# Kernel tuning notes

Hardware: AMD Instinct MI355X
Metric: run time of the kernel (lower is better)

Reference implementation:

```python
import jax, jax.numpy as jnp
import numpy as np

P = 2        # patch_size
HEADS = 1


def _conv(x, w, b, groups=1):
    # NCHW conv, kernel 3x3, SAME padding (stride 1)
    y = jax.lax.conv_general_dilated(
        x, w, window_strides=(1, 1), padding='SAME',
        dimension_numbers=('NCHW', 'OIHW', 'NCHW'),
        feature_group_count=groups)
    return y + b[None, :, None, None]


def _unfold(x, p):
    # torch.nn.Unfold(kernel=p, stride=p): [B,C,h,w] -> [B, C*p*p, n]
    B, C, h, w = x.shape
    x = x.reshape(B, C, h // p, p, w // p, p)
    x = x.transpose(0, 1, 3, 5, 2, 4)  # (B, C, ph, pw, h/p, w/p)
    return x.reshape(B, C * p * p, (h // p) * (w // p))


def _fold(x, p, h, w):
    # inverse of _unfold (non-overlapping patches)
    B = x.shape[0]
    C = x.shape[1] // (p * p)
    x = x.reshape(B, C, p, p, h // p, w // p)
    x = x.transpose(0, 1, 4, 2, 5, 3)  # (B, C, h/p, ph, w/p, pw)
    return x.reshape(B, C, h, w)


def setup_inputs() -> dict:
    key = jax.random.key(0)
    ks = jax.random.split(key, 9)
    c = 64
    x = jax.random.normal(ks[0], (2, 5, c, 64, 64), jnp.float32)
    wq = jax.random.normal(ks[1], (c, 1, 3, 3), jnp.float32) * 0.1
    bq = jax.random.normal(ks[2], (c,), jnp.float32) * 0.1
    wk = jax.random.normal(ks[3], (c, 1, 3, 3), jnp.float32) * 0.1
    bk = jax.random.normal(ks[4], (c,), jnp.float32) * 0.1
    wv = jax.random.normal(ks[5], (c, c, 3, 3), jnp.float32) * 0.05
    bv = jax.random.normal(ks[6], (c,), jnp.float32) * 0.1
    wc = jax.random.normal(ks[7], (c, c, 3, 3), jnp.float32) * 0.05
    bc = jax.random.normal(ks[8], (c,), jnp.float32) * 0.1
    return {"x": x, "wq": wq, "bq": bq, "wk": wk, "bk": bk,
            "wv": wv, "bv": bv, "wc": wc, "bc": bc}


def reference(x, wq, bq, wk, bk, wv, bv, wc, bc):
    b, t, c, h, w = x.shape
    p, H = P, HEADS
    D = p * p * c           # 256
    d = D // H              # per-head dim
    n = (h // p) * (w // p)  # tokens per frame

    xf = x.reshape(b * t, c, h, w)
    q = _conv(xf, wq, bq, groups=c)   # depthwise
    k = _conv(xf, wk, bk, groups=c)   # depthwise
    v = _conv(xf, wv, bv)             # dense conv

    def to_tokens(y):
        # [bt, D, n] -> [b, H, d, t*n]
        u = _unfold(y, p).reshape(b, t, H, d, n)
        return u.transpose(0, 2, 3, 1, 4).reshape(b, H, d, t * n)

    uq, uk, uv = to_tokens(q), to_tokens(k), to_tokens(v)

    attn = jnp.einsum('bhdi,bhdj->bhij', uq, uk) * (d ** -0.5)
    attn = jax.nn.softmax(attn, axis=-1)           # [b,H,tn,tn]
    ax = jnp.einsum('bhij,bhdj->bhid', attn, uv)   # [b,H,tn,d]

    ax = ax.reshape(b, H, t, n, d).transpose(0, 2, 1, 4, 3).reshape(b * t, D, n)
    feat = _fold(ax, p, h, w)                      # [bt, c, h, w]
    out = _conv(feat, wc, bc).reshape(x.shape) + x
    return out
```

## Files before the change

kernel.cpp:

```cpp
#include <hip/hip_runtime.h>
#include <hip/hip_bf16.h>

typedef __attribute__((ext_vector_type(8))) short short8;
typedef __attribute__((ext_vector_type(8))) unsigned short ushort8;
typedef __attribute__((ext_vector_type(4))) unsigned short ushort4v;
typedef __attribute__((ext_vector_type(4))) float f32x4;

#define NTOK 5120
#define DDIM 256
#define NJC 8

__device__ __forceinline__ unsigned short f2bf(float f) {
  union { float f; unsigned int u; } x; x.f = f;
  unsigned int r = x.u + 0x7FFFu + ((x.u >> 16) & 1u);
  return (unsigned short)(r >> 16);
}
__device__ __forceinline__ float bf2f(unsigned short u) {
  union { unsigned int i; float f; } x; x.i = ((unsigned int)u) << 16; return x.f;
}

__global__ __launch_bounds__(256) void qk_gen(
    const float* __restrict__ xin, const float* __restrict__ wq,
    const float* __restrict__ bq, const float* __restrict__ wk,
    const float* __restrict__ bk, unsigned short* __restrict__ qt,
    unsigned short* __restrict__ kt)
{
  const int ch = blockIdx.x;
  const int bt = blockIdx.y;
  const int b = bt / 5, tf = bt % 5;
  const int tid = threadIdx.x;
  const float* xp = xin + ((size_t)bt * 64 + ch) * 4096;
  float wqv[9], wkv[9];
  #pragma unroll
  for (int i = 0; i < 9; i++) { wqv[i] = wq[ch * 9 + i]; wkv[i] = wk[ch * 9 + i]; }
  const float bqv = bq[ch], bkv = bk[ch];

  #pragma unroll
  for (int p = 0; p < 4; p++) {
    int pid = tid + p * 256;
    int gy = pid >> 5, gx = pid & 31;
    float v[4][4];
    #pragma unroll
    for (int r = 0; r < 4; r++) {
      int yy = 2 * gy - 1 + r;
      #pragma unroll
      for (int cc = 0; cc < 4; cc++) {
        int xx = 2 * gx - 1 + cc;
        bool ok = (yy >= 0) && (yy < 64) && (xx >= 0) && (xx < 64);
        v[r][cc] = ok ? xp[yy * 64 + xx] : 0.f;
      }
    }
    unsigned short qo[4], ko[4];
    #pragma unroll
    for (int py = 0; py < 2; py++)
      #pragma unroll
      for (int px = 0; px < 2; px++) {
        float aq = bqv, ak = bkv;
        #pragma unroll
        for (int dy = 0; dy < 3; dy++)
          #pragma unroll
          for (int dx = 0; dx < 3; dx++) {
            float xv = v[py + dy][px + dx];
            aq += wqv[dy * 3 + dx] * xv;
            ak += wkv[dy * 3 + dx] * xv;
          }
        qo[py * 2 + px] = f2bf(aq);
        ko[py * 2 + px] = f2bf(ak);
      }
    size_t base = ((size_t)(b * NTOK + tf * 1024 + pid)) * DDIM + ch * 4;
    ushort4v qv = { qo[0], qo[1], qo[2], qo[3] };
    ushort4v kv = { ko[0], ko[1], ko[2], ko[3] };
    *(ushort4v*)(qt + base) = qv;
    *(ushort4v*)(kt + base) = kv;
  }
}

__global__ __launch_bounds__(256) void wt_gen(
    const float* __restrict__ w0, const float* __restrict__ w1,
    unsigned short* __restrict__ o0, unsigned short* __restrict__ o1)
{
  const int tap = blockIdx.x;
  const float* src = blockIdx.y ? w1 : w0;
  unsigned short* dst = blockIdx.y ? o1 : o0;
  const int t = threadIdx.x;
  #pragma unroll
  for (int i = 0; i < 16; i++) {
    int oi = t + i * 256;
    dst[tap * 4096 + oi] = f2bf(src[(size_t)oi * 9 + tap]);
  }
}

template<int MODE>
__global__ __launch_bounds__(256) void conv_mfma(
    const float* __restrict__ src, const unsigned short* __restrict__ wt,
    const float* __restrict__ bias, const float* __restrict__ resid,
    float* __restrict__ dstf, unsigned short* __restrict__ vt)
{
  const int strip = blockIdx.x;
  const int bt = blockIdx.y;
  const int y0 = strip * 2;
  const int tid = threadIdx.x;
  const int sw = tid >> 6, lane = tid & 63;
  const int ry = sw >> 1, ch = sw & 1;
  const int g = lane >> 4, c = lane & 15;

  __shared__ __align__(16) unsigned short lds_in[4 * 66 * 64];
  __shared__ __align__(16) unsigned short lds_w[64 * 64];

  {
    const int rr = lane >> 4;
    const int cb = lane & 15;
    const int row = y0 - 1 + rr;
    const bool rok = (row >= 0) && (row < 64);
    #pragma unroll
    for (int pp = 0; pp < 8; ++pp) {
      const int ci0 = sw * 16 + pp * 2;
      f32x4 va = { 0.f, 0.f, 0.f, 0.f }, vb = { 0.f, 0.f, 0.f, 0.f };
      if (rok) {
        va = *(const f32x4*)(src + ((size_t)(bt * 64 + ci0)) * 4096 + row * 64 + cb * 4);
        vb = *(const f32x4*)(src + ((size_t)(bt * 64 + ci0 + 1)) * 4096 + row * 64 + cb * 4);
      }
      char* rbase = (char*)lds_in + (rr * 66) * 128 + (ci0 & 7) * 2;
      const int sl = ci0 >> 3;
      #pragma unroll
      for (int q = 0; q < 4; ++q) {
        int lcol = cb * 4 + q + 1;
        unsigned int pk = (unsigned int)f2bf(va[q]) | ((unsigned int)f2bf(vb[q]) << 16);
        *(unsigned int*)(rbase + lcol * 128 + ((sl ^ (lcol & 7)) * 16)) = pk;
      }
      if (cb == 0)  *(unsigned int*)(rbase + ((sl ^ 0) * 16)) = 0u;
      if (cb == 15) *(unsigned int*)(rbase + 65 * 128 + ((sl ^ 1) * 16)) = 0u;
    }
  }

  f32x4 acc[2][4];
  #pragma unroll
  for (int ct = 0; ct < 2; ct++)
    #pragma unroll
    for (int xt = 0; xt < 4; xt++) acc[ct][xt] = (f32x4){ 0.f, 0.f, 0.f, 0.f };

  #pragma unroll 1
  for (int tap = 0; tap < 9; ++tap) {
    __syncthreads();
    {
      const unsigned short* wp = wt + tap * 4096;
      #pragma unroll
      for (int h = 0; h < 2; ++h) {
        int el = h * 2048 + tid * 8;
        int co = el >> 6, sl = (el & 63) >> 3;
        short8 wv8 = *(const short8*)(wp + el);
        *(short8*)((char*)lds_w + co * 128 + ((sl ^ (co & 7)) * 16)) = wv8;
      }
    }
    __syncthreads();
    const int dy = tap / 3 - 1, dx = tap % 3 - 1;
    const int rowp = ry + 1 + dy;
    #pragma unroll
    for (int kblk = 0; kblk < 2; ++kblk) {
      short8 af[2], bf[4];
      #pragma unroll
      for (int ct = 0; ct < 2; ++ct) {
        int co = ch * 32 + ct * 16 + c;
        af[ct] = *(const short8*)((char*)lds_w + co * 128 + (((kblk * 4 + g) ^ (co & 7)) * 16));
      }
      #pragma unroll
      for (int xt = 0; xt < 4; ++xt) {
        int lcol = xt * 16 + c + dx + 1;
        bf[xt] = *(const short8*)((char*)lds_in + (rowp * 66 + lcol) * 128 + (((kblk * 4 + g) ^ (lcol & 7)) * 16));
      }
      #pragma unroll
      for (int ct = 0; ct < 2; ++ct)
        #pragma unroll
        for (int xt = 0; xt < 4; ++xt)
          acc[ct][xt] = __builtin_amdgcn_mfma_f32_16x16x32_bf16(af[ct], bf[xt], acc[ct][xt], 0, 0, 0);
    }
  }

  const int y = y0 + ry;
  if (MODE == 0) {
    const int b = bt / 5, tf = bt % 5;
    const int py = y & 1, gy = y >> 1;
    #pragma unroll
    for (int ct = 0; ct < 2; ++ct)
      #pragma unroll
      for (int r = 0; r < 4; ++r) {
        const int co = ch * 32 + ct * 16 + g * 4 + r;
        const float bv = bias[co];
        #pragma unroll
        for (int xt = 0; xt < 4; ++xt) {
          int x = xt * 16 + c;
          int d = co * 4 + py * 2 + (x & 1);
          int tok = tf * 1024 + gy * 32 + (x >> 1);
          vt[((size_t)(b * DDIM + d)) * NTOK + tok] = f2bf(acc[ct][xt][r] + bv);
        }
      }
  } else {
    #pragma unroll
    for (int ct = 0; ct < 2; ++ct)
      #pragma unroll
      for (int r = 0; r < 4; ++r) {
        const int co = ch * 32 + ct * 16 + g * 4 + r;
        const float bv = bias[co];
        const size_t rowb = ((size_t)(bt * 64 + co)) * 4096 + (size_t)y * 64;
        #pragma unroll
        for (int xt = 0; xt < 4; ++xt) {
          int x = xt * 16 + c;
          dstf[rowb + x] = acc[ct][xt][r] + bv + resid[rowb + x];
        }
      }
  }
}

__global__ __launch_bounds__(256) void attn_kernel(
    const unsigned short* __restrict__ qt, const unsigned short* __restrict__ kt,
    const unsigned short* __restrict__ vt, float* __restrict__ po,
    float* __restrict__ pm, float* __restrict__ pl)
{
  const int wgid = blockIdx.x;
  const int chunk = wgid / 320;
  const int within = wgid % 320;
  const int slice = chunk * 8 + (within & 7);
  const int b = slice >> 3;
  const int jc = slice & 7;
  const int i0 = (within >> 3) * 128;
  const int jchunk = NTOK / NJC;
  const int tid = threadIdx.x;
  const int w = tid >> 6, lane = tid & 63;
  const int g = lane >> 4, c = lane & 15;

  __shared__ __align__(16) unsigned short lds_k[2][64 * 256];
  __shared__ __align__(16) unsigned short lds_v[2][256 * 64];
  __shared__ __align__(16) unsigned short lds_p[4 * 16 * 64];

  const float C2 = 0.0625f * 1.4426950408889634f;

  short8 qf[2][8];
  #pragma unroll
  for (int st = 0; st < 2; st++) {
    const unsigned short* qr = qt + ((size_t)(b * NTOK + i0 + w * 32 + st * 16 + c)) * DDIM + g * 8;
    #pragma unroll
    for (int kb = 0; kb < 8; kb++) qf[st][kb] = *(const short8*)(qr + kb * 32);
  }
  f32x4 o[32];
  #pragma unroll
  for (int i = 0; i < 32; i++) o[i] = (f32x4){ 0.f, 0.f, 0.f, 0.f };
  float m[2][4], l[2][4];
  #pragma unroll
  for (int st = 0; st < 2; st++)
    #pragma unroll
    for (int r = 0; r < 4; r++) { m[st][r] = -1e30f; l[st][r] = 0.f; }

  const int sr = tid >> 5, sc = tid & 31;
  const int vdr = tid >> 3, vcc = tid & 7;
  char* pb = (char*)lds_p + w * 2048;

  const int jbeg = jc * jchunk;
  const int jend = jbeg + jchunk;

  {
    #pragma unroll
    for (int p = 0; p < 8; p++) {
      int row = sr + p * 8;
      short8 kv = *(const short8*)(kt + ((size_t)(b * NTOK + jbeg + row)) * DDIM + sc * 8);
      *(short8*)((char*)lds_k[0] + row * 512 + ((sc ^ (row & 7)) * 16)) = kv;
      int dd = vdr + p * 32;
      short8 vv = *(const short8*)(vt + ((size_t)(b * DDIM + dd)) * NTOK + jbeg + vcc * 8);
      *(short8*)((char*)lds_v[0] + dd * 128 + ((vcc ^ (dd & 7)) * 16)) = vv;
    }
  }
  __syncthreads();

  int cur = 0;
  for (int j0 = jbeg; j0 < jend; j0 += 64) {
    const bool more = (j0 + 64 < jend);

    f32x4 s0[4], s1[4];
    #pragma unroll
    for (int js = 0; js < 4; js++) {
      s0[js] = (f32x4){ 0.f, 0.f, 0.f, 0.f };
      s1[js] = (f32x4){ 0.f, 0.f, 0.f, 0.f };
      int row = js * 16 + c;
      int sw2 = row & 7;
      #pragma unroll
      for (int kb = 0; kb < 8; kb++) {
        short8 kf = *(const short8*)((char*)lds_k[cur] + row * 512 + (((kb * 4 + g) ^ sw2) * 16));
        s0[js] = __builtin_amdgcn_mfma_f32_16x16x32_bf16(qf[0][kb], kf, s0[js], 0, 0, 0);
        s1[js] = __builtin_amdgcn_mfma_f32_16x16x32_bf16(qf[1][kb], kf, s1[js], 0, 0, 0);
      }
    }

    short8 kpre[8], vpre[8];
    if (more) {
      const int jn = j0 + 64;
      #pragma unroll
      for (int p = 0; p < 8; p++) {
        int row = sr + p * 8;
        kpre[p] = *(const short8*)(kt + ((size_t)(b * NTOK + jn + row)) * DDIM + sc * 8);
        int dd = vdr + p * 32;
        vpre[p] = *(const short8*)(vt + ((size_t)(b * DDIM + dd)) * NTOK + jn + vcc * 8);
      }
    }

    short8 pf[2][2];
    {
      float pvv[4][4], alpha[4];
      #pragma unroll
      for (int r = 0; r < 4; r++) {
        float t0 = s0[0][r] * C2, t1 = s0[1][r] * C2, t2 = s0[2][r] * C2, t3 = s0[3][r] * C2;
        float mx = fmaxf(fmaxf(t0, t1), fmaxf(t2, t3));
        #pragma unroll
        for (int off = 1; off < 16; off <<= 1) mx = fmaxf(mx, __shfl_xor(mx, off));
        float mn = fmaxf(m[0][r], mx);
        alpha[r] = exp2f(m[0][r] - mn);
        float p0 = exp2f(t0 - mn);
        float p1 = exp2f(t1 - mn);
        float p2 = exp2f(t2 - mn);
        float p3 = exp2f(t3 - mn);
        pvv[0][r] = p0; pvv[1][r] = p1; pvv[2][r] = p2; pvv[3][r] = p3;
        float sum = p0 + p1 + p2 + p3;
        #pragma unroll
        for (int off = 1; off < 16; off <<= 1) sum += __shfl_xor(sum, off);
        l[0][r] = l[0][r] * alpha[r] + sum;
        m[0][r] = mn;
      }
      f32x4 av = { alpha[0], alpha[1], alpha[2], alpha[3] };
      #pragma unroll
      for (int ds = 0; ds < 16; ds++) o[ds] *= av;
      #pragma unroll
      for (int js = 0; js < 4; js++)
        #pragma unroll
        for (int r = 0; r < 4; r++) {
          int row = 4 * g + r;
          int slot = (js * 2 + (c >> 3)) ^ (row & 7);
          *(unsigned short*)(pb + row * 128 + slot * 16 + (c & 7) * 2) = f2bf(pvv[js][r]);
        }
      #pragma unroll
      for (int k2 = 0; k2 < 2; k2++)
        pf[0][k2] = *(short8*)(pb + c * 128 + (((k2 * 4 + g) ^ (c & 7)) * 16));
    }
    {
      float pvv[4][4], alpha[4];
      #pragma unroll
      for (int r = 0; r < 4; r++) {
        float t0 = s1[0][r] * C2, t1 = s1[1][r] * C2, t2 = s1[2][r] * C2, t3 = s1[3][r] * C2;
        float mx = fmaxf(fmaxf(t0, t1), fmaxf(t2, t3));
        #pragma unroll
        for (int off = 1; off < 16; off <<= 1) mx = fmaxf(mx, __shfl_xor(mx, off));
        float mn = fmaxf(m[1][r], mx);
        alpha[r] = exp2f(m[1][r] - mn);
        float p0 = exp2f(t0 - mn);
        float p1 = exp2f(t1 - mn);
        float p2 = exp2f(t2 - mn);
        float p3 = exp2f(t3 - mn);
        pvv[0][r] = p0; pvv[1][r] = p1; pvv[2][r] = p2; pvv[3][r] = p3;
        float sum = p0 + p1 + p2 + p3;
        #pragma unroll
        for (int off = 1; off < 16; off <<= 1) sum += __shfl_xor(sum, off);
        l[1][r] = l[1][r] * alpha[r] + sum;
        m[1][r] = mn;
      }
      f32x4 av = { alpha[0], alpha[1], alpha[2], alpha[3] };
      #pragma unroll
      for (int ds = 0; ds < 16; ds++) o[16 + ds] *= av;
      #pragma unroll
      for (int js = 0; js < 4; js++)
        #pragma unroll
        for (int r = 0; r < 4; r++) {
          int row = 4 * g + r;
          int slot = (js * 2 + (c >> 3)) ^ (row & 7);
          *(unsigned short*)(pb + row * 128 + slot * 16 + (c & 7) * 2) = f2bf(pvv[js][r]);
        }
      #pragma unroll
      for (int k2 = 0; k2 < 2; k2++)
        pf[1][k2] = *(short8*)(pb + c * 128 + (((k2 * 4 + g) ^ (c & 7)) * 16));
    }

    if (more) {
      #pragma unroll
      for (int p = 0; p < 8; p++) {
        int row = sr + p * 8;
        *(short8*)((char*)lds_k[cur ^ 1] + row * 512 + ((sc ^ (row & 7)) * 16)) = kpre[p];
        int dd = vdr + p * 32;
        *(short8*)((char*)lds_v[cur ^ 1] + dd * 128 + ((vcc ^ (dd & 7)) * 16)) = vpre[p];
      }
    }

    #pragma unroll
    for (int ds = 0; ds < 16; ds++) {
      int vrow = ds * 16 + c;
      int sw2 = c & 7;
      #pragma unroll
      for (int k2 = 0; k2 < 2; k2++) {
        short8 vf = *(const short8*)((char*)lds_v[cur] + vrow * 128 + (((k2 * 4 + g) ^ sw2) * 16));
        o[ds]      = __builtin_amdgcn_mfma_f32_16x16x32_bf16(pf[0][k2], vf, o[ds], 0, 0, 0);
        o[16 + ds] = __builtin_amdgcn_mfma_f32_16x16x32_bf16(pf[1][k2], vf, o[16 + ds], 0, 0, 0);
      }
    }
    __syncthreads();
    cur ^= 1;
  }
  #pragma unroll
  for (int st = 0; st < 2; st++) {
    const size_t rbase = ((size_t)(b * NJC + jc)) * NTOK + i0 + w * 32 + st * 16;
    #pragma unroll
    for (int ds = 0; ds < 16; ds++)
      #pragma unroll
      for (int r = 0; r < 4; r++)
        po[(rbase + 4 * g + r) * DDIM + ds * 16 + c] = o[st * 16 + ds][r];
    if (c == 0) {
      #pragma unroll
      for (int r = 0; r < 4; r++) {
        pm[rbase + 4 * g + r] = m[st][r];
        pl[rbase + 4 * g + r] = l[st][r];
      }
    }
  }
}

__global__ __launch_bounds__(256) void attn_combine(
    const float* __restrict__ po, const float* __restrict__ pm,
    const float* __restrict__ pl, float* __restrict__ feat, int njc)
{
  const int b = blockIdx.y;
  const int i0 = blockIdx.x * 64;
  const int t = threadIdx.x;
  const int row = t >> 2, dq = (t & 3) * 64;
  const int i = i0 + row;

  float M = -1e30f, L = 0.f;
  f32x4 acc[16];
  #pragma unroll
  for (int q = 0; q < 16; q++) acc[q] = (f32x4){ 0.f, 0.f, 0.f, 0.f };

  #pragma unroll 1
  for (int jc = 0; jc < njc; jc++) {
    const size_t rb = ((size_t)(b * njc + jc)) * NTOK + i;
    float mj = pm[rb], lj = pl[rb];
    float mn = fmaxf(M, mj);
    float so = exp2f(M - mn), sn = exp2f(mj - mn);
    const float* pp = po + rb * DDIM + dq;
    #pragma unroll
    for (int q = 0; q < 16; q++) {
      f32x4 v = *(const f32x4*)(pp + q * 4);
      acc[q] = acc[q] * so + v * sn;
    }
    L = L * so + lj * sn;
    M = mn;
  }
  const float inv = 1.f / L;
  const int tf = i >> 10, jn = i & 1023;
  const int gy = jn >> 5, gx = jn & 31;
  const size_t fb = ((size_t)((b * 5 + tf) * 64)) * 4096 + (2 * gy) * 64 + 2 * gx;
  #pragma unroll
  for (int q = 0; q < 16; q++) {
    f32x4 a = acc[q] * inv;
    int ch = (dq + q * 4) >> 2;
    size_t base = fb + (size_t)ch * 4096;
    feat[base] = a[0]; feat[base + 1] = a[1];
    feat[base + 64] = a[2]; feat[base + 65] = a[3];
  }
}

extern "C" void kernel_launch(void* const* d_in, const int* in_sizes, int n_in,
                              void* d_out, int out_size, void* d_ws, size_t ws_size,
                              hipStream_t stream) {
  const float* x  = (const float*)d_in[0];
  const float* wq = (const float*)d_in[1];
  const float* bq = (const float*)d_in[2];
  const float* wk = (const float*)d_in[3];
  const float* bk = (const float*)d_in[4];
  const float* wv = (const float*)d_in[5];
  const float* bv = (const float*)d_in[6];
  const float* wc = (const float*)d_in[7];
  const float* bc = (const float*)d_in[8];
  float* out = (float*)d_out;

  char* ws = (char*)d_ws;
  unsigned short* qt = (unsigned short*)(ws);
  unsigned short* kt = (unsigned short*)(ws + 5242880);
  unsigned short* vt = (unsigned short*)(ws + 10485760);
  float*          ft = (float*)(ws + 15728640);
  unsigned short* wtv = (unsigned short*)(ws + 26214400);
  unsigned short* wtc = (unsigned short*)(ws + 26288128);
  const size_t big_off = 26361856;
  float* po = (float*)(ws + big_off);

  size_t po_bytes = (size_t)2 * NJC * NTOK * DDIM * 4;
  float* pm = (float*)(ws + big_off + po_bytes);
  float* pl = pm + (size_t)2 * NJC * NTOK;

  wt_gen        <<<dim3(9, 2), 256, 0, stream>>>(wv, wc, wtv, wtc);
  qk_gen        <<<dim3(64, 10), 256, 0, stream>>>(x, wq, bq, wk, bk, qt, kt);
  conv_mfma<0>  <<<dim3(32, 10), 256, 0, stream>>>(x, wtv, bv, nullptr, nullptr, vt);
  attn_kernel   <<<dim3(640), 256, 0, stream>>>(qt, kt, vt, po, pm, pl);
  attn_combine  <<<dim3(80, 2), 256, 0, stream>>>(po, pm, pl, ft, NJC);
  conv_mfma<1>  <<<dim3(32, 10), 256, 0, stream>>>(ft, wtc, bc, x, out, nullptr);
}
```

Measured before the change: 270.6 us.

## Stage K/V tiles with direct global-to-LDS loads instead of register round-trip

Replaces the register-staged prefetch of K and V tiles (global load into registers, then LDS store after softmax) with global_load_lds async copies that write straight into the double-buffered LDS tiles. The inverse swizzle is applied on the global address so each wave's contiguous LDS destination matches the XOR layout the MFMA reads expect. This frees 16 short8 registers per thread and removes explicit LDS stores, which could ease register pressure and improve overlap. The risk is that ordering now depends on the existing __syncthreads and waitcnt handling, and the address mapping must match the wave-contiguous write pattern of the intrinsic.

```diff
diff --git a/kernel.cpp b/kernel.cpp
--- a/kernel.cpp
+++ b/kernel.cpp
@@ -17,6 +17,12 @@
 }
 __device__ __forceinline__ float bf2f(unsigned short u) {
   union { unsigned int i; float f; } x; x.i = ((unsigned int)u) << 16; return x.f;
+}
+
+__device__ __forceinline__ void gload16(const unsigned short* g, unsigned short* l) {
+  __builtin_amdgcn_global_load_lds(
+      (const __attribute__((address_space(1))) void*)g,
+      (__attribute__((address_space(3))) void*)l, 16, 0, 0);
 }
 
 __global__ __launch_bounds__(256) void qk_gen(
@@ -257,22 +263,28 @@
   const int jbeg = jc * jchunk;
   const int jend = jbeg + jchunk;
 
-  {
+  auto stage = [&](int j0, int bb) {
+    const unsigned short* kbase = kt + ((size_t)b * NTOK + j0) * DDIM;
+    const unsigned short* vbase = vt + (size_t)b * DDIM * NTOK + j0;
     #pragma unroll
     for (int p = 0; p < 8; p++) {
       int row = sr + p * 8;
-      short8 kv = *(const short8*)(kt + ((size_t)(b * NTOK + jbeg + row)) * DDIM + sc * 8);
-      *(short8*)((char*)lds_k[0] + row * 512 + ((sc ^ (row & 7)) * 16)) = kv;
+      int col16 = sc ^ (row & 7);
+      gload16(kbase + (size_t)row * DDIM + col16 * 8,
+              &lds_k[bb][(w * 2 + p * 8) * 256]);
       int dd = vdr + p * 32;
-      short8 vv = *(const short8*)(vt + ((size_t)(b * DDIM + dd)) * NTOK + jbeg + vcc * 8);
-      *(short8*)((char*)lds_v[0] + dd * 128 + ((vcc ^ (dd & 7)) * 16)) = vv;
-    }
-  }
+      int colblk = vcc ^ (dd & 7);
+      gload16(vbase + (size_t)dd * NTOK + colblk * 8,
+              &lds_v[bb][(w * 8 + p * 32) * 64]);
+    }
+  };
+
+  stage(jbeg, 0);
   __syncthreads();
 
   int cur = 0;
   for (int j0 = jbeg; j0 < jend; j0 += 64) {
-    const bool more = (j0 + 64 < jend);
+    if (j0 + 64 < jend) stage(j0 + 64, cur ^ 1);
 
     f32x4 s0[4], s1[4];
     #pragma unroll
@@ -288,19 +300,6 @@
         s1[js] = __builtin_amdgcn_mfma_f32_16x16x32_bf16(qf[1][kb], kf, s1[js], 0, 0, 0);
       }
     }
-
-    short8 kpre[8], vpre[8];
-    if (more) {
-      const int jn = j0 + 64;
-      #pragma unroll
-      for (int p = 0; p < 8; p++) {
-        int row = sr + p * 8;
-        kpre[p] = *(const short8*)(kt + ((size_t)(b * NTOK + jn + row)) * DDIM + sc * 8);
-        int dd = vdr + p * 32;
-        vpre[p] = *(const short8*)(vt + ((size_t)(b * DDIM + dd)) * NTOK + jn + vcc * 8);
-      }
-    }
-
     short8 pf[2][2];
     {
       float pvv[4][4], alpha[4];
@@ -374,17 +373,6 @@
       for (int k2 = 0; k2 < 2; k2++)
         pf[1][k2] = *(short8*)(pb + c * 128 + (((k2 * 4 + g) ^ (c & 7)) * 16));
     }
-
-    if (more) {
-      #pragma unroll
-      for (int p = 0; p < 8; p++) {
-        int row = sr + p * 8;
-        *(short8*)((char*)lds_k[cur ^ 1] + row * 512 + ((sc ^ (row & 7)) * 16)) = kpre[p];
-        int dd = vdr + p * 32;
-        *(short8*)((char*)lds_v[cur ^ 1] + dd * 128 + ((vcc ^ (dd & 7)) * 16)) = vpre[p];
-      }
-    }
-
     #pragma unroll
     for (int ds = 0; ds < 16; ds++) {
       int vrow = ds * 16 + c;
```

Result: slower. 285.0 us (+5.3%).
